# Kernel optimization log

Measured on AMD Instinct MI355X. Metric: run time of the kernel, lower is better.

Reference implementation:

```python
import jax, jax.numpy as jnp
import numpy as np

B, L, C = 2, 1024, 512
H, P = 8, 4
D = C // H
LN_EPS = 1e-5


def setup_inputs() -> dict:
    key = jax.random.key(0)
    ks = jax.random.split(key, 12)
    s = 0.02
    inp = {
        "features": jax.random.normal(ks[0], (B, L, C), jnp.float32),
        "coords": jax.random.normal(ks[1], (B, L, 3), jnp.float32),
        # LayerNorm params
        "ln_g": jnp.ones((C,), jnp.float32),
        "ln_b": jnp.zeros((C,), jnp.float32),
        # scalar q/k/v projections (stored as [in, out])
        "wq": jax.random.normal(ks[2], (C, C), jnp.float32) * s,
        "bq": jnp.zeros((C,), jnp.float32),
        "wk": jax.random.normal(ks[3], (C, C), jnp.float32) * s,
        "bk": jnp.zeros((C,), jnp.float32),
        "wv": jax.random.normal(ks[4], (C, C), jnp.float32) * s,
        "bv": jnp.zeros((C,), jnp.float32),
        # point q/k/v projections: [C, H*P*3]
        "wqp": jax.random.normal(ks[5], (C, H * P * 3), jnp.float32) * s,
        "bqp": jnp.zeros((H * P * 3,), jnp.float32),
        "wkp": jax.random.normal(ks[6], (C, H * P * 3), jnp.float32) * s,
        "bkp": jnp.zeros((H * P * 3,), jnp.float32),
        "wvp": jax.random.normal(ks[7], (C, H * P * 3), jnp.float32) * s,
        "bvp": jnp.zeros((H * P * 3,), jnp.float32),
        # output projection
        "wo": jax.random.normal(ks[8], (C, C), jnp.float32) * s,
        "bo": jnp.zeros((C,), jnp.float32),
        # per-head point scale, init 1/sqrt(P)
        "pscale": jnp.full((H,), 1.0 / np.sqrt(P), jnp.float32),
    }
    return inp


def _layernorm(x, g, b):
    mu = jnp.mean(x, axis=-1, keepdims=True)
    var = jnp.mean((x - mu) ** 2, axis=-1, keepdims=True)
    return (x - mu) * jax.lax.rsqrt(var + LN_EPS) * g + b


def reference(features, coords, ln_g, ln_b, wq, bq, wk, bk, wv, bv,
              wqp, bqp, wkp, bkp, wvp, bvp, wo, bo, pscale):
    b, l, c = features.shape
    h = pscale.shape[0]
    d = c // h
    p = wqp.shape[1] // (h * 3)

    x = _layernorm(features, ln_g, ln_b)

    # scalar heads: [b,h,l,d]
    q_s = (x @ wq + bq).reshape(b, l, h, d).transpose(0, 2, 1, 3)
    k_s = (x @ wk + bk).reshape(b, l, h, d).transpose(0, 2, 1, 3)
    v_s = (x @ wv + bv).reshape(b, l, h, d).transpose(0, 2, 1, 3)

    # point heads: [b,h,l,p,3]
    q_p = (x @ wqp + bqp).reshape(b, l, h, p, 3).transpose(0, 2, 1, 3, 4)
    k_p = (x @ wkp + bkp).reshape(b, l, h, p, 3).transpose(0, 2, 1, 3, 4)

    # scalar logits
    logits_s = jnp.einsum('bhid,bhjd->bhij', q_s, k_s) * (d ** -0.5)

    # point-distance logits: sum_{p,k} ||q - k||^2 = |q|^2 + |k|^2 - 2 q.k
    # (avoids materializing the [b,h,l,l,p,3] difference tensor)
    dot = jnp.einsum('bhipk,bhjpk->bhij', q_p, k_p)
    qsq = jnp.sum(q_p * q_p, axis=(-1, -2))  # [b,h,l]
    ksq = jnp.sum(k_p * k_p, axis=(-1, -2))  # [b,h,l]
    pdist2 = qsq[..., :, None] + ksq[..., None, :] - 2.0 * dot  # [b,h,l,l]

    logits = logits_s - pdist2 * pscale[None, :, None, None]

    attn = jax.nn.softmax(logits, axis=-1)  # dropout is identity in eval

    out_s = jnp.einsum('bhij,bhjd->bhid', attn, v_s)
    out_s = out_s.transpose(0, 2, 1, 3).reshape(b, l, c)

    out = out_s @ wo + bo  # out_dropout is identity in eval
    return out
```

## Files before the change

kernel.cpp:

```cpp
#include <hip/hip_runtime.h>
#include <math.h>

#define BB 2
#define LL 1024
#define CCH 512
#define HH 8
#define LN_EPSF 1e-5f

typedef short s16x8 __attribute__((ext_vector_type(8)));
typedef float fx4 __attribute__((ext_vector_type(4)));


__device__ __forceinline__ unsigned short f2bf(float f) {
  unsigned u = __float_as_uint(f);
  unsigned r = (u + 0x7FFFu + ((u >> 16) & 1u)) >> 16;
  return (unsigned short)r;
}
__device__ __forceinline__ float bf2f(unsigned short h) {
  return __uint_as_float(((unsigned)h) << 16);
}
__device__ __forceinline__ s16x8 ldfrag(const unsigned short* p) {
  int4 t = *(const int4*)p;
  return *(s16x8*)&t;
}

template <int CTRL>
__device__ __forceinline__ float dpp_mov(float x) {
  return __int_as_float(
      __builtin_amdgcn_update_dpp(0, __float_as_int(x), CTRL, 0xF, 0xF, true));
}
__device__ __forceinline__ float red16_sum(float v) {
  v += dpp_mov<0x121>(v);
  v += dpp_mov<0x122>(v);
  v += dpp_mov<0x124>(v);
  v += dpp_mov<0x128>(v);
  return v;
}
__device__ __forceinline__ float red16_max(float v) {
  v = fmaxf(v, dpp_mov<0x121>(v));
  v = fmaxf(v, dpp_mov<0x122>(v));
  v = fmaxf(v, dpp_mov<0x124>(v));
  v = fmaxf(v, dpp_mov<0x128>(v));
  return v;
}
__device__ __forceinline__ float wave_sum(float v) {
  v = red16_sum(v);
  v += __shfl_xor(v, 16);
  v += __shfl_xor(v, 32);
  return v;
}

__global__ __launch_bounds__(256) void prep(
    const float* __restrict__ f, const float* __restrict__ g,
    const float* __restrict__ bta, unsigned short* __restrict__ xh,
    unsigned short* __restrict__ xl, const float* __restrict__ wq,
    const float* __restrict__ wk, const float* __restrict__ wv,
    const float* __restrict__ wo, const float* __restrict__ wqp,
    const float* __restrict__ wkp, unsigned short* __restrict__ wt_h,
    unsigned short* __restrict__ qt, unsigned short* __restrict__ kt_,
    float* __restrict__ out) {
  __shared__ unsigned short lh[64][68];
  __shared__ float red[8];
  const int tid = threadIdx.x;
  const int bxg = blockIdx.x;
  if (bxg < 2048) {
    const int row = bxg;
    const int wave = tid >> 6, lane = tid & 63;
    const float* fr = f + (size_t)row * CCH;
    float2 v = *(const float2*)&fr[tid * 2];
    float s = wave_sum(v.x + v.y);
    if (lane == 0) red[wave] = s;
    __syncthreads();
    float mu = (red[0] + red[1] + red[2] + red[3]) * (1.0f / CCH);
    float dx = v.x - mu, dy = v.y - mu;
    float sq = wave_sum(dx * dx + dy * dy);
    if (lane == 0) red[4 + wave] = sq;
    __syncthreads();
    float var = (red[4] + red[5] + red[6] + red[7]) * (1.0f / CCH);
    float inv = 1.0f / sqrtf(var + LN_EPSF);
    float2 gg = *(const float2*)&g[tid * 2];
    float2 bb = *(const float2*)&bta[tid * 2];
    float ox = dx * inv * gg.x + bb.x;
    float oy = dy * inv * gg.y + bb.y;
    unsigned short h0 = f2bf(ox), h1 = f2bf(oy);
    ushort2 hv; hv.x = h0; hv.y = h1;
    ushort2 lv; lv.x = f2bf(ox - bf2f(h0)); lv.y = f2bf(oy - bf2f(h1));
    const int k0c = tid * 2;
    size_t addr = ((size_t)((row >> 4) * 16 + (k0c >> 5))) * 512 +
                  (((k0c >> 3) & 3) * 16 + (row & 15)) * 8 + (k0c & 7);
    *(ushort2*)&xh[addr] = hv;
    *(ushort2*)&xl[addr] = lv;
  } else if (bxg < 2336) {
    const int bx = bxg - 2048;
    const float* W;
    int Ncols, rowbase, kt, nt;
    if (bx < 256) {
      int mat = bx >> 6, t = bx & 63;
      kt = t >> 3; nt = t & 7; Ncols = 512;
      if (mat == 0) { W = wq; rowbase = 0; }
      else if (mat == 1) { W = wk; rowbase = 512; }
      else if (mat == 2) { W = wv; rowbase = 1024; }
      else { W = wo; rowbase = 1536; }
    } else {
      int r = bx - 256; int mat = r >> 4; int t = r & 15;
      kt = t >> 1; nt = t & 1; Ncols = 96;
      if (mat == 0) { W = wqp; rowbase = 2048; }
      else { W = wkp; rowbase = 2144; }
    }
    const int k0 = kt * 64, n0 = nt * 64;
    const int c = tid & 63;
#pragma unroll
    for (int ii = 0; ii < 16; ++ii) {
      int r = ii * 4 + (tid >> 6);
      float val = (n0 + c < Ncols) ? W[(size_t)(k0 + r) * Ncols + n0 + c] : 0.f;
      lh[r][c] = f2bf(val);
    }
    __syncthreads();
    const int base_nt = (rowbase >> 4) + (n0 >> 4);
    const int base_kt = (k0 >> 5);
#pragma unroll
    for (int cc = 0; cc < 2; ++cc) {
      int ch = cc * 256 + tid;
      int lane2 = ch & 63, ktl = (ch >> 6) & 1, ntl = ch >> 7;
      int l16c = lane2 & 15, quadc = lane2 >> 4;
      if (n0 + ntl * 16 < Ncols) {
        unsigned short th[8] __attribute__((aligned(16)));
#pragma unroll
        for (int jj = 0; jj < 8; ++jj)
          th[jj] = lh[ktl * 32 + quadc * 8 + jj][ntl * 16 + l16c];
        *(int4*)&wt_h[((size_t)((base_nt + ntl) * 16 + base_kt + ktl)) * 512 +
                      lane2 * 8] = *(int4*)th;
      }
    }
  } else if (bxg < 2400) {
    const int vb2 = bxg - 2336;
    const int4 zero = {0, 0, 0, 0};
    for (int u = tid; u < 32 * 48; u += 256) {
      int t = u / 48, off = (u - t * 48) * 8;
      int gidx = vb2 * 32 + t;
      unsigned short* dst = (gidx < 1024) ? qt : kt_;
      int rem = gidx & 1023;
      int bh = rem >> 6, lt = rem & 63;
      size_t base = ((size_t)(bh * 64 + lt) * 3 + 2) * 512;
      *(int4*)&dst[base + 128 + off] = zero;
    }
  } else {
    const int vb3 = bxg - 2400;
    const float4 zero = {0.f, 0.f, 0.f, 0.f};
    float4* dst = (float4*)(out + (size_t)vb3 * 4096);
#pragma unroll
    for (int i = 0; i < 4; ++i) dst[i * 256 + tid] = zero;
  }
}

template <int MF, int NF, int TERMS>
__device__ __forceinline__ void mfma_core_frag(
    const unsigned short* __restrict__ Ah, const unsigned short* __restrict__ Al,
    const unsigned short* __restrict__ Bt, int mt0, int ntbase, int nt0,
    int ntmax, int ks0, int ks1, fx4 acc[MF][NF]) {
  const int lane = threadIdx.x & 63;
  int bt[NF];
#pragma unroll
  for (int j = 0; j < NF; ++j) {
    int nt = nt0 + j;
    if (nt > ntmax) nt = ntmax;
    bt[j] = ntbase + nt;
  }
#pragma unroll
  for (int i = 0; i < MF; ++i)
#pragma unroll
    for (int j = 0; j < NF; ++j) acc[i][j] = (fx4){0.f, 0.f, 0.f, 0.f};
  for (int ks = ks0; ks < ks1; ++ks) {
    s16x8 ah[MF], al[MF], b[NF];
#pragma unroll
    for (int i = 0; i < MF; ++i) {
      size_t off = ((size_t)((mt0 + i) * 16 + ks)) * 512 + lane * 8;
      ah[i] = ldfrag(&Ah[off]);
      if (TERMS == 2) al[i] = ldfrag(&Al[off]);
    }
#pragma unroll
    for (int j = 0; j < NF; ++j)
      b[j] = ldfrag(&Bt[((size_t)(bt[j] * 16 + ks)) * 512 + lane * 8]);
#pragma unroll
    for (int i = 0; i < MF; ++i)
#pragma unroll
      for (int j = 0; j < NF; ++j) {
        acc[i][j] = __builtin_amdgcn_mfma_f32_16x16x32_bf16(ah[i], b[j], acc[i][j], 0, 0, 0);
        if (TERMS == 2)
          acc[i][j] = __builtin_amdgcn_mfma_f32_16x16x32_bf16(al[i], b[j], acc[i][j], 0, 0, 0);
      }
  }
}

__global__ __launch_bounds__(256, 4) void proj_mfma(
    const unsigned short* __restrict__ xh, const unsigned short* __restrict__ xl,
    const unsigned short* __restrict__ wt_h,
    const float* __restrict__ bq, const float* __restrict__ bk,
    const float* __restrict__ bv, const float* __restrict__ bqp,
    const float* __restrict__ bkp, const float* __restrict__ pscale,
    unsigned short* __restrict__ qt, unsigned short* __restrict__ kt_,
    unsigned short* __restrict__ vth) {
  __shared__ unsigned short vt_lds[64][72];
  const int bx = blockIdx.x;
  const int m0 = blockIdx.y * 64;
  const int tid = threadIdx.x;
  const int wave = __builtin_amdgcn_readfirstlane(tid >> 6);
  const int lane = tid & 63;
  const int quad = lane >> 4, l16 = lane & 15;
  const int mw = m0 + (wave & 1) * 32;
  const int mt0 = mw >> 4;

  if (bx < 16) {
    const bool isq = bx < 8;
    const float* bias = isq ? bq : bk;
    unsigned short* pdst = isq ? qt : kt_;
    const int n0 = (bx & 7) * 64;
    const int nw = n0 + (wave >> 1) * 32;
    fx4 acc[2][2];
    mfma_core_frag<2, 2, 1>(xh, xh, wt_h, mt0, isq ? 0 : 32, nw >> 4, 31, 0, 16, acc);
#pragma unroll
    for (int j = 0; j < 2; ++j) {
      int n = nw + j * 16 + l16;
      int h = n >> 6, d = n & 63;
      float bb = bias[n];
#pragma unroll
      for (int i = 0; i < 2; ++i)
#pragma unroll
        for (int reg = 0; reg < 4; ++reg) {
          int row = mw + i * 16 + quad * 4 + reg;
          int bi = row >> 10, l = row & 1023;
          int bh2 = bi * 8 + h;
          float val = (acc[i][j][reg] + bb) * 0.35355339059f;
          size_t tile = ((size_t)(bh2 * 64 + (l >> 4))) * 3 + (d >> 5);
          pdst[tile * 512 + (((d >> 3) & 3) * 16 + (l & 15)) * 8 + (d & 7)] = f2bf(val);
        }
    }
  } else if (bx < 24) {
    const int h = bx - 16;
    const int nw = h * 64 + (wave >> 1) * 32;
    fx4 acc[2][2];
    mfma_core_frag<2, 2, 2>(xh, xl, wt_h, mt0, 64, nw >> 4, 31, 0, 16, acc);
#pragma unroll
    for (int j = 0; j < 2; ++j) {
      int dl = (wave >> 1) * 32 + j * 16 + l16;
      float bb = bv[h * 64 + dl];
#pragma unroll
      for (int i = 0; i < 2; ++i)
#pragma unroll
        for (int reg = 0; reg < 4; ++reg) {
          int lm = (wave & 1) * 32 + i * 16 + quad * 4 + reg;
          vt_lds[lm][dl] = f2bf(acc[i][j][reg] + bb);
        }
    }
    __syncthreads();
    const int b = m0 >> 10, l0 = m0 & 1023;
    const int bh2 = b * 8 + h;
#pragma unroll
    for (int cc = 0; cc < 2; ++cc) {
      int ch = cc * 256 + tid;
      int lane2 = ch & 63, jt = (ch >> 6) & 1, ft = ch >> 7;
      int l16c = lane2 & 15, quadc = lane2 >> 4;
      unsigned short th[8] __attribute__((aligned(16)));
#pragma unroll
      for (int jj = 0; jj < 8; ++jj)
        th[jj] = vt_lds[jt * 32 + quadc * 8 + jj][ft * 16 + l16c];
      size_t tile = ((size_t)(bh2 * 4 + ft)) * 32 + (l0 >> 5) + jt;
      *(int4*)&vth[tile * 512 + lane2 * 8] = *(int4*)th;
    }
  } else {
    const bool isq = bx < 26;
    const float* bias = isq ? bqp : bkp;
    unsigned short* pdst = isq ? qt : kt_;
    const int n0 = (bx & 1) * 64;
    const int nw = n0 + (wave >> 1) * 32;
    fx4 acc[2][2];
    mfma_core_frag<2, 2, 1>(xh, xh, wt_h, mt0, isq ? 128 : 134, nw >> 4, 5, 0, 16, acc);
#pragma unroll
    for (int j = 0; j < 2; ++j) {
      int n = nw + j * 16 + l16;
      bool ok = n < 96;
      int nn = ok ? n : 0;
      int h = nn / 12, c = nn - h * 12;
      float sc = sqrtf(2.f * pscale[h]);
      float bb = bias[nn];
#pragma unroll
      for (int i = 0; i < 2; ++i)
#pragma unroll
        for (int reg = 0; reg < 4; ++reg) {
          int row = mw + i * 16 + quad * 4 + reg;
          int bi = row >> 10, l = row & 1023;
          int bh2 = bi * 8 + h;
          float val = (acc[i][j][reg] + bb) * sc;
          if (ok) {
            int kc = 64 + c;
            size_t tile = ((size_t)(bh2 * 64 + (l >> 4))) * 3 + 2;
            pdst[tile * 512 + (((kc >> 3) & 3) * 16 + (l & 15)) * 8 + (kc & 7)] =
                f2bf(val);
          }
        }
    }
  }
}

__global__ __launch_bounds__(256, 4) void out_proj_mfma(
    const unsigned short* __restrict__ oh,
    const unsigned short* __restrict__ wt_h, const float* __restrict__ bo,
    float* __restrict__ out) {
  const int tid = threadIdx.x;
  const int wave = __builtin_amdgcn_readfirstlane(tid >> 6);
  const int lane = tid & 63;
  const int quad = lane >> 4, l16 = lane & 15;
  const int mw = blockIdx.y * 64 + (wave & 1) * 32;
  const int nw = blockIdx.x * 64 + (wave >> 1) * 32;
  const int kz = blockIdx.z;
  fx4 acc[2][2];
  mfma_core_frag<2, 2, 1>(oh, oh, wt_h, mw >> 4, 96, nw >> 4, 31, kz * 4,
                          kz * 4 + 4, acc);
#pragma unroll
  for (int j = 0; j < 2; ++j) {
    int n = nw + j * 16 + l16;
    float bb = (kz == 0) ? bo[n] : 0.f;
#pragma unroll
    for (int i = 0; i < 2; ++i)
#pragma unroll
      for (int reg = 0; reg < 4; ++reg) {
        int row = mw + i * 16 + quad * 4 + reg;
        atomicAdd(&out[(size_t)row * 512 + n], acc[i][j][reg] + bb);
      }
  }
}

__global__ __launch_bounds__(512, 4) void ipa_attn_mfma(
    const unsigned short* __restrict__ qt, const unsigned short* __restrict__ kt_,
    const unsigned short* __restrict__ vth, unsigned short* __restrict__ oh) {
  const int bid = blockIdx.x;
  const int low3 = bid & 7;
  const int slot = bid >> 3;
  const int qtile = slot & 31;
  const int bh = ((slot >> 5) << 3) | low3;
  const int tid = threadIdx.x;
  const int wave = tid >> 6, lane = tid & 63;
  const int quad = lane >> 4, l16 = lane & 15;
  const int mstrip = wave & 1, kq = wave >> 1;
  const int ibase = qtile * 32 + mstrip * 16;

  __shared__ unsigned short pb[8][16][32];
  __shared__ float obuf[8][16][64];
  __shared__ float mred[8][16], lred[8][16];
  __shared__ float qsl[8][16];

  s16x8 aq[3];
#pragma unroll
  for (int s = 0; s < 3; ++s)
    aq[s] = ldfrag(&qt[(((size_t)(bh * 64 + (ibase >> 4))) * 3 + s) * 512 + lane * 8]);

  {
    float qp = 0.f;
#pragma unroll
    for (int j = 0; j < 8; ++j) {
      float v = bf2f((unsigned short)aq[2][j]);
      qp += v * v;
    }
    qp += __shfl_xor(qp, 16);
    qp += __shfl_xor(qp, 32);
    qsl[wave][l16] = 0.5f * qp;
  }
  float qs_r[4];
#pragma unroll
  for (int reg = 0; reg < 4; ++reg) qs_r[reg] = qsl[wave][quad * 4 + reg];

  fx4 o[4];
#pragma unroll
  for (int f = 0; f < 4; ++f) o[f] = (fx4){0.f, 0.f, 0.f, 0.f};
  float m_r[4], l_r[4];
#pragma unroll
  for (int reg = 0; reg < 4; ++reg) { m_r[reg] = -INFINITY; l_r[reg] = 0.f; }

#pragma unroll 1
  for (int c = 0; c < 8; ++c) {
    const int j0 = kq * 256 + c * 32;
    s16x8 bk[2][3];
#pragma unroll
    for (int f = 0; f < 2; ++f)
#pragma unroll
      for (int s = 0; s < 3; ++s)
        bk[f][s] = ldfrag(
            &kt_[(((size_t)(bh * 64 + (j0 >> 4) + f)) * 3 + s) * 512 + lane * 8]);
    s16x8 bvh[4];
#pragma unroll
    for (int f = 0; f < 4; ++f)
      bvh[f] = ldfrag(
          &vth[(((size_t)(bh * 4 + f)) * 32 + (j0 >> 5)) * 512 + lane * 8]);

    float kp0 = 0.f, kp1 = 0.f;
#pragma unroll
    for (int j = 0; j < 8; ++j) {
      float v0 = bf2f((unsigned short)bk[0][2][j]);
      float v1 = bf2f((unsigned short)bk[1][2][j]);
      kp0 += v0 * v0;
      kp1 += v1 * v1;
    }
    kp0 += __shfl_xor(kp0, 16);
    kp0 += __shfl_xor(kp0, 32);
    kp1 += __shfl_xor(kp1, 16);
    kp1 += __shfl_xor(kp1, 32);
    float ks0 = 0.5f * kp0, ks1 = 0.5f * kp1;

    fx4 sa[2];
    sa[0] = (fx4){0.f, 0.f, 0.f, 0.f};
    sa[1] = (fx4){0.f, 0.f, 0.f, 0.f};
#pragma unroll
    for (int f = 0; f < 2; ++f)
#pragma unroll
      for (int s = 0; s < 3; ++s)
        sa[f] = __builtin_amdgcn_mfma_f32_16x16x32_bf16(aq[s], bk[f][s], sa[f], 0, 0, 0);

#pragma unroll
    for (int reg = 0; reg < 4; ++reg) {
      float z0 = sa[0][reg] - qs_r[reg] - ks0;
      float z1 = sa[1][reg] - qs_r[reg] - ks1;
      float mx = red16_max(fmaxf(z0, z1));
      float mnew = fmaxf(m_r[reg], mx);
      float p0 = __expf(z0 - mnew), p1 = __expf(z1 - mnew);
      float alpha = __expf(m_r[reg] - mnew);
      float psum = red16_sum(p0 + p1);
      l_r[reg] = l_r[reg] * alpha + psum;
      m_r[reg] = mnew;
      o[0][reg] *= alpha; o[1][reg] *= alpha; o[2][reg] *= alpha; o[3][reg] *= alpha;
      pb[wave][quad * 4 + reg][l16] = f2bf(p0);
      pb[wave][quad * 4 + reg][16 + l16] = f2bf(p1);
    }
    s16x8 ap = ldfrag(&pb[wave][l16][quad * 8]);
#pragma unroll
    for (int f = 0; f < 4; ++f)
      o[f] = __builtin_amdgcn_mfma_f32_16x16x32_bf16(ap, bvh[f], o[f], 0, 0, 0);
  }
  if (l16 == 0) {
#pragma unroll
    for (int reg = 0; reg < 4; ++reg) {
      mred[wave][quad * 4 + reg] = m_r[reg];
      lred[wave][quad * 4 + reg] = l_r[reg];
    }
  }
#pragma unroll
  for (int f = 0; f < 4; ++f)
#pragma unroll
    for (int reg = 0; reg < 4; ++reg)
      obuf[wave][quad * 4 + reg][f * 16 + l16] = o[f][reg];
  __syncthreads();
  if (kq == 0) {
    const int b = bh >> 3, h = bh & 7;
#pragma unroll
    for (int f = 0; f < 4; ++f)
#pragma unroll
      for (int reg = 0; reg < 4; ++reg) {
        int row = quad * 4 + reg;
        int d = f * 16 + l16;
        float M = -INFINITY;
#pragma unroll
        for (int p = 0; p < 4; ++p) M = fmaxf(M, mred[wave + p * 2][row]);
        float L = 0.f, val = 0.f;
#pragma unroll
        for (int p = 0; p < 4; ++p) {
          float w = __expf(mred[wave + p * 2][row] - M);
          L += lred[wave + p * 2][row] * w;
          val += obuf[wave + p * 2][row][d] * w;
        }
        val /= L;
        int m = b * LL + ibase + row;
        int kcol = h * 64 + d;
        size_t tile = ((size_t)(m >> 4)) * 16 + (kcol >> 5);
        oh[tile * 512 + (((kcol >> 3) & 3) * 16 + (m & 15)) * 8 + (kcol & 7)] =
            f2bf(val);
      }
  }
}

extern "C" void kernel_launch(void* const* d_in, const int* in_sizes, int n_in,
                              void* d_out, int out_size, void* d_ws, size_t ws_size,
                              hipStream_t stream) {
  (void)in_sizes; (void)n_in; (void)out_size; (void)ws_size;
  const float* features = (const float*)d_in[0];
  const float* ln_g = (const float*)d_in[2];
  const float* ln_b = (const float*)d_in[3];
  const float* wq = (const float*)d_in[4];
  const float* bq = (const float*)d_in[5];
  const float* wk = (const float*)d_in[6];
  const float* bk = (const float*)d_in[7];
  const float* wv = (const float*)d_in[8];
  const float* bv = (const float*)d_in[9];
  const float* wqp = (const float*)d_in[10];
  const float* bqp = (const float*)d_in[11];
  const float* wkp = (const float*)d_in[12];
  const float* bkp = (const float*)d_in[13];
  const float* wo = (const float*)d_in[16];
  const float* bo = (const float*)d_in[17];
  const float* pscale = (const float*)d_in[18];
  float* out = (float*)d_out;

  char* cur = (char*)d_ws;
  const size_t NTOK = (size_t)BB * LL;
  unsigned short* xh = (unsigned short*)cur; cur += NTOK * CCH * 2;
  unsigned short* xl = (unsigned short*)cur; cur += NTOK * CCH * 2;
  unsigned short* wt_h = (unsigned short*)cur; cur += (size_t)2240 * 512 * 2;
  unsigned short* qt = (unsigned short*)cur; cur += (size_t)16 * LL * 96 * 2;
  unsigned short* kt_ = (unsigned short*)cur; cur += (size_t)16 * LL * 96 * 2;
  unsigned short* vth = (unsigned short*)cur; cur += (size_t)16 * 64 * LL * 2;
  unsigned short* oh = (unsigned short*)cur; cur += NTOK * CCH * 2;

  prep<<<dim3(2656), 256, 0, stream>>>(features, ln_g, ln_b, xh, xl, wq, wk, wv,
                                       wo, wqp, wkp, wt_h, qt, kt_, out);
  proj_mfma<<<dim3(28, 32), 256, 0, stream>>>(xh, xl, wt_h, bq, bk, bv, bqp, bkp,
                                              pscale, qt, kt_, vth);
  ipa_attn_mfma<<<dim3(512), 512, 0, stream>>>(qt, kt_, vth, oh);
  out_proj_mfma<<<dim3(8, 32, 4), 256, 0, stream>>>(oh, wt_h, bo, out);
}
```

Baseline: 155.5 us.

## Fuse output projection into attention epilogue with per-head atomic accumulation

Removes the separate out_proj kernel and the bf16 intermediate buffer `oh`. Each attention block now stages its normalized 32x64 head output in LDS, reusing the `pb` scratch. All eight waves then multiply it by that head's slice of the output weights with MFMA and atomically add into the fp32 output; the bias is added only by the head-0 blocks. This saves one kernel launch and a global write and read of the attention output. In exchange it doubles the atomic adds per output element (eight heads instead of four K-splits) and adds weight loads and an extra barrier to the attention kernel's tail.

New measurement: 164.3 us. +5.7%, slower.

```diff
diff --git a/kernel.cpp b/kernel.cpp
--- a/kernel.cpp
+++ b/kernel.cpp
@@ -302,37 +302,10 @@
   }
 }
 
-__global__ __launch_bounds__(256, 4) void out_proj_mfma(
-    const unsigned short* __restrict__ oh,
-    const unsigned short* __restrict__ wt_h, const float* __restrict__ bo,
-    float* __restrict__ out) {
-  const int tid = threadIdx.x;
-  const int wave = __builtin_amdgcn_readfirstlane(tid >> 6);
-  const int lane = tid & 63;
-  const int quad = lane >> 4, l16 = lane & 15;
-  const int mw = blockIdx.y * 64 + (wave & 1) * 32;
-  const int nw = blockIdx.x * 64 + (wave >> 1) * 32;
-  const int kz = blockIdx.z;
-  fx4 acc[2][2];
-  mfma_core_frag<2, 2, 1>(oh, oh, wt_h, mw >> 4, 96, nw >> 4, 31, kz * 4,
-                          kz * 4 + 4, acc);
-#pragma unroll
-  for (int j = 0; j < 2; ++j) {
-    int n = nw + j * 16 + l16;
-    float bb = (kz == 0) ? bo[n] : 0.f;
-#pragma unroll
-    for (int i = 0; i < 2; ++i)
-#pragma unroll
-      for (int reg = 0; reg < 4; ++reg) {
-        int row = mw + i * 16 + quad * 4 + reg;
-        atomicAdd(&out[(size_t)row * 512 + n], acc[i][j][reg] + bb);
-      }
-  }
-}
-
 __global__ __launch_bounds__(512, 4) void ipa_attn_mfma(
     const unsigned short* __restrict__ qt, const unsigned short* __restrict__ kt_,
-    const unsigned short* __restrict__ vth, unsigned short* __restrict__ oh) {
+    const unsigned short* __restrict__ vth, const unsigned short* __restrict__ wt_h,
+    const float* __restrict__ bo, float* __restrict__ out) {
   const int bid = blockIdx.x;
   const int low3 = bid & 7;
   const int slot = bid >> 3;
@@ -448,8 +421,9 @@
     for (int reg = 0; reg < 4; ++reg)
       obuf[wave][quad * 4 + reg][f * 16 + l16] = o[f][reg];
   __syncthreads();
+
+  unsigned short* plds = (unsigned short*)pb;
   if (kq == 0) {
-    const int b = bh >> 3, h = bh & 7;
 #pragma unroll
     for (int f = 0; f < 4; ++f)
 #pragma unroll
@@ -467,12 +441,50 @@
           val += obuf[wave + p * 2][row][d] * w;
         }
         val /= L;
-        int m = b * LL + ibase + row;
-        int kcol = h * 64 + d;
-        size_t tile = ((size_t)(m >> 4)) * 16 + (kcol >> 5);
-        oh[tile * 512 + (((kcol >> 3) & 3) * 16 + (m & 15)) * 8 + (kcol & 7)] =
-            f2bf(val);
+        plds[(mstrip * 16 + row) * 72 + d] = f2bf(val);
       }
+  }
+  __syncthreads();
+
+  {
+    const int b = bh >> 3, h = bh & 7;
+    const int i0 = qtile * 32;
+    const int nt0 = wave * 4;
+    fx4 acc[2][4];
+#pragma unroll
+    for (int i = 0; i < 2; ++i)
+#pragma unroll
+      for (int j = 0; j < 4; ++j) acc[i][j] = (fx4){0.f, 0.f, 0.f, 0.f};
+#pragma unroll
+    for (int kt2 = 0; kt2 < 2; ++kt2) {
+      s16x8 a[2];
+#pragma unroll
+      for (int i = 0; i < 2; ++i)
+        a[i] = ldfrag(&plds[(i * 16 + l16) * 72 + kt2 * 32 + quad * 8]);
+      s16x8 bfrag[4];
+#pragma unroll
+      for (int j = 0; j < 4; ++j)
+        bfrag[j] = ldfrag(&wt_h[((size_t)((96 + nt0 + j) * 16 + h * 2 + kt2)) * 512 +
+                                lane * 8]);
+#pragma unroll
+      for (int i = 0; i < 2; ++i)
+#pragma unroll
+        for (int j = 0; j < 4; ++j)
+          acc[i][j] = __builtin_amdgcn_mfma_f32_16x16x32_bf16(a[i], bfrag[j],
+                                                              acc[i][j], 0, 0, 0);
+    }
+#pragma unroll
+    for (int j = 0; j < 4; ++j) {
+      int n = (nt0 + j) * 16 + l16;
+      float bb = (h == 0) ? bo[n] : 0.f;
+#pragma unroll
+      for (int i = 0; i < 2; ++i)
+#pragma unroll
+        for (int reg = 0; reg < 4; ++reg) {
+          int token = b * LL + i0 + i * 16 + quad * 4 + reg;
+          atomicAdd(&out[(size_t)token * 512 + n], acc[i][j][reg] + bb);
+        }
+    }
   }
 }
 
@@ -506,12 +518,10 @@
   unsigned short* qt = (unsigned short*)cur; cur += (size_t)16 * LL * 96 * 2;
   unsigned short* kt_ = (unsigned short*)cur; cur += (size_t)16 * LL * 96 * 2;
   unsigned short* vth = (unsigned short*)cur; cur += (size_t)16 * 64 * LL * 2;
-  unsigned short* oh = (unsigned short*)cur; cur += NTOK * CCH * 2;
 
   prep<<<dim3(2656), 256, 0, stream>>>(features, ln_g, ln_b, xh, xl, wq, wk, wv,
                                        wo, wqp, wkp, wt_h, qt, kt_, out);
   proj_mfma<<<dim3(28, 32), 256, 0, stream>>>(xh, xl, wt_h, bq, bk, bv, bqp, bkp,
                                               pscale, qt, kt_, vth);
-  ipa_attn_mfma<<<dim3(512), 512, 0, stream>>>(qt, kt_, vth, oh);
-  out_proj_mfma<<<dim3(8, 32, 4), 256, 0, stream>>>(oh, wt_h, bo, out);
-}
+  ipa_attn_mfma<<<dim3(512), 512, 0, stream>>>(qt, kt_, vth, wt_h, bo, out);
+}
```
